# Optimization experiments

Hardware: AMD Instinct MI355X
Metric: run time of the kernel (lower is better)

Reference implementation:

```python
import jax, jax.numpy as jnp
import numpy as np

N = 50000
E = 800000
H = 128

def _mlp_init(key, sizes, bias_flags):
    ws = []
    for i, (din, dout) in enumerate(zip(sizes[:-1], sizes[1:])):
        key, k1, k2 = jax.random.split(key, 3)
        lim = 1.0 / np.sqrt(din)
        W = jax.random.uniform(k1, (din, dout), jnp.float32, -lim, lim)
        ws.append(W)
        if bias_flags[i]:
            ws.append(jax.random.uniform(k2, (dout,), jnp.float32, -lim, lim))
    return key, ws

def setup_inputs() -> dict:
    key = jax.random.key(0)
    key, kh, kx, ke = jax.random.split(key, 4)
    h = jax.random.normal(kh, (N, H), jnp.float32)
    x = jax.random.normal(kx, (N, 3), jnp.float32)
    edge_index = jax.random.randint(ke, (2, E), 0, N, jnp.int64)
    # edge_mlp: Linear(2H+1, H), Linear(H, H), both with bias
    key, (W_e1, b_e1, W_e2, b_e2) = _mlp_init(key, [2 * H + 1, H, H], [True, True])
    # coord_mlp: Linear(H, H) with bias, Linear(H, 1) no bias
    key, (W_c1, b_c1, W_c2) = _mlp_init(key, [H, H, 1], [True, False])
    # node_mlp: Linear(2H, H), Linear(H, H), both with bias
    key, (W_n1, b_n1, W_n2, b_n2) = _mlp_init(key, [2 * H, H, H], [True, True])
    ln_g = jnp.ones((H,), jnp.float32)
    ln_b = jnp.zeros((H,), jnp.float32)
    return {"h": h, "x": x, "edge_index": edge_index,
            "W_e1": W_e1, "b_e1": b_e1, "W_e2": W_e2, "b_e2": b_e2,
            "W_c1": W_c1, "b_c1": b_c1, "W_c2": W_c2,
            "W_n1": W_n1, "b_n1": b_n1, "W_n2": W_n2, "b_n2": b_n2,
            "ln_g": ln_g, "ln_b": ln_b}

def reference(h, x, edge_index, W_e1, b_e1, W_e2, b_e2, W_c1, b_c1, W_c2,
              W_n1, b_n1, W_n2, b_n2, ln_g, ln_b):
    row, col = edge_index[0], edge_index[1]
    coord_diff = x[row] - x[col]                       # [E, 3]
    dist = jnp.linalg.norm(coord_diff, axis=1, keepdims=True)  # [E, 1]
    radial = dist ** 2
    edge_input = jnp.concatenate([h[row], h[col], radial], axis=1)  # [E, 2H+1]
    m_ij = jax.nn.silu(jax.nn.silu(edge_input @ W_e1 + b_e1) @ W_e2 + b_e2)  # [E, H]
    force_scalar = jnp.tanh(jax.nn.silu(m_ij @ W_c1 + b_c1) @ W_c2) * 0.1    # [E, 1]
    norm_diff = coord_diff / (dist + 1e-8)
    force_vector = norm_diff * force_scalar            # [E, 3]
    x_new = x + jax.ops.segment_sum(force_vector, row, num_segments=N)
    m_i = jax.ops.segment_sum(m_ij, row, num_segments=N)  # [N, H]
    node_input = jnp.concatenate([h, m_i], axis=1)     # [N, 2H]
    h_res = h + jax.nn.silu(node_input @ W_n1 + b_n1) @ W_n2 + b_n2
    mu = jnp.mean(h_res, axis=-1, keepdims=True)
    var = jnp.var(h_res, axis=-1, keepdims=True)
    h_new = (h_res - mu) / jnp.sqrt(var + 1e-5) * ln_g + ln_b
    return (h_new, x_new)
```

## Files before the change

### kernel.cpp

```cpp
#include <hip/hip_runtime.h>
#include <hip/hip_bf16.h>

#define NN 50000
#define NE 800000
#define HH 128
#define SCAN_NB 196

typedef short s16x8 __attribute__((ext_vector_type(8)));
typedef float f32x4 __attribute__((ext_vector_type(4)));
typedef unsigned int u32x4 __attribute__((ext_vector_type(4)));
typedef __bf16 bf16x2 __attribute__((ext_vector_type(2)));

__device__ __forceinline__ float u2f(unsigned int v) {
    float f;
    __builtin_memcpy(&f, &v, 4);
    return f;
}
__device__ __forceinline__ float bf2f(unsigned short u) {
    return u2f(((unsigned int)u) << 16);
}
__device__ __forceinline__ unsigned short f2bf_sw(float f) {
    unsigned int x;
    __builtin_memcpy(&x, &f, 4);
    unsigned int r = (x + 0x7fffu + ((x >> 16) & 1u)) >> 16;
    return (unsigned short)r;
}
__device__ __forceinline__ unsigned int f2bf_pk(float a, float b) {
#if __has_builtin(__builtin_amdgcn_cvt_pk_bf16_f32)
    bf16x2 p = __builtin_amdgcn_cvt_pk_bf16_f32(a, b);
    unsigned int u;
    __builtin_memcpy(&u, &p, 4);
    return u;
#else
    return (unsigned int)f2bf_sw(a) | ((unsigned int)f2bf_sw(b) << 16);
#endif
}
__device__ __forceinline__ unsigned short f2bf(float a) {
#if __has_builtin(__builtin_amdgcn_cvt_pk_bf16_f32)
    return (unsigned short)(f2bf_pk(a, a) & 0xffffu);
#else
    return f2bf_sw(a);
#endif
}
__device__ __forceinline__ float silu(float v) {
    return v * __builtin_amdgcn_rcpf(1.f + __expf(-v));
}

__global__ void prep_kernel(
    const float* __restrict__ W_e1, const float* __restrict__ W_e2,
    const float* __restrict__ W_c1, const float* __restrict__ W_n1,
    const float* __restrict__ W_n2, const int* __restrict__ eidx,
    unsigned short* __restrict__ PWT, unsigned short* __restrict__ W2T,
    unsigned short* __restrict__ Wc1T, unsigned short* __restrict__ Wn1T,
    unsigned short* __restrict__ Wn2T, int* __restrict__ counts) {
    int idx = blockIdx.x * 256 + threadIdx.x;
    if (idx < 32768) {
        int cp = idx >> 7, k = idx & 127;
        int srow = (cp < 128) ? k : (128 + k);
        PWT[idx] = f2bf(W_e1[srow * 128 + (cp & 127)]);
    } else if (idx < 49152) {
        int i = idx - 32768, n = i >> 7, k = i & 127;
        W2T[i] = f2bf(W_e2[k * 128 + n]);
    } else if (idx < 65536) {
        int i = idx - 49152, n = i >> 7, k = i & 127;
        Wc1T[i] = f2bf(W_c1[k * 128 + n]);
    } else if (idx < 98304) {
        int i = idx - 65536, n = i >> 8, k = i & 255;
        Wn1T[i] = f2bf(W_n1[k * 128 + n]);
    } else if (idx < 114688) {
        int i = idx - 98304, n = i >> 7, k = i & 127;
        Wn2T[i] = f2bf(W_n2[k * 128 + n]);
    } else if (idx < 114688 + NE) {
        int e = idx - 114688;
        int r = eidx[e];
        r = r < 0 ? 0 : (r >= NN ? NN - 1 : r);
        atomicAdd(&counts[r], 1);
    }
}

__global__ void k_partial(const int* __restrict__ counts, int* __restrict__ partials) {
    __shared__ int sm[256];
    int idx = blockIdx.x * 256 + threadIdx.x;
    sm[threadIdx.x] = idx < NN ? counts[idx] : 0;
    __syncthreads();
    for (int s = 128; s > 0; s >>= 1) {
        if (threadIdx.x < s) sm[threadIdx.x] += sm[threadIdx.x + s];
        __syncthreads();
    }
    if (threadIdx.x == 0) partials[blockIdx.x] = sm[0];
}
__global__ void k_scanp(const int* __restrict__ partials, int* __restrict__ scanp) {
    __shared__ int sm[256];
    int t = threadIdx.x;
    int v = t < SCAN_NB ? partials[t] : 0;
    sm[t] = v;
    __syncthreads();
    for (int d = 1; d < 256; d <<= 1) {
        int add = t >= d ? sm[t - d] : 0;
        __syncthreads();
        sm[t] += add;
        __syncthreads();
    }
    scanp[t] = sm[t] - v;
}
__global__ void k_offsets(const int* __restrict__ counts, const int* __restrict__ scanp,
                          int* __restrict__ offsets) {
    __shared__ int sm[256];
    int t = threadIdx.x, idx = blockIdx.x * 256 + t;
    int v = idx < NN ? counts[idx] : 0;
    sm[t] = v;
    __syncthreads();
    for (int d = 1; d < 256; d <<= 1) {
        int add = t >= d ? sm[t - d] : 0;
        __syncthreads();
        sm[t] += add;
        __syncthreads();
    }
    if (idx < NN) offsets[idx] = sm[t] - v + scanp[blockIdx.x];
}

__global__ void k_fill(const int* __restrict__ eidx, const int* __restrict__ offsets,
                       int* __restrict__ cursor, unsigned int* __restrict__ rc) {
    int e = blockIdx.x * 256 + threadIdx.x;
    if (e >= NE) return;
    int r = eidx[e];
    int c = eidx[NE + e];
    r = r < 0 ? 0 : (r >= NN ? NN - 1 : r);
    c = c < 0 ? 0 : (c >= NN ? NN - 1 : c);
    int slot = offsets[r] + atomicAdd(&cursor[r], 1);
    rc[slot] = (unsigned int)r | ((unsigned int)c << 16);
}

__global__ __launch_bounds__(256, 4) void pgemm(
    const float* __restrict__ h, const unsigned short* __restrict__ PWT,
    const float* __restrict__ b1,
    float* __restrict__ P1, unsigned short* __restrict__ P2b) {
    __shared__ unsigned short Alds[64 * 136];
    const int tid = threadIdx.x;
    const int n0 = blockIdx.x * 64;

#pragma unroll
    for (int j = 0; j < 4; j++) {
        int idx = tid + j * 256;
        int e = idx >> 4, ch = idx & 15;
        int node = n0 + e;
        if (node >= NN) node = NN - 1;
        const f32x4* p = (const f32x4*)&h[node * 128 + ch * 8];
        f32x4 a = p[0], b = p[1];
        u32x4 s;
        s[0] = f2bf_pk(a[0], a[1]);
        s[1] = f2bf_pk(a[2], a[3]);
        s[2] = f2bf_pk(b[0], b[1]);
        s[3] = f2bf_pk(b[2], b[3]);
        *(u32x4*)&Alds[e * 136 + ch * 8] = s;
    }
    __syncthreads();

    const int lane = tid & 63;
    const int w = tid >> 6;
    const int ln15 = lane & 15;
    const int q8 = (lane >> 4) * 8, q4 = (lane >> 4) * 4;
    const int cbase = w * 64;

    f32x4 acc[4][4];
#pragma unroll
    for (int et = 0; et < 4; et++)
#pragma unroll
        for (int nt = 0; nt < 4; nt++) acc[et][nt] = (f32x4){0.f, 0.f, 0.f, 0.f};
#pragma unroll
    for (int kk = 0; kk < 4; kk++) {
        int k0 = kk * 32 + q8;
        s16x8 a[4], b[4];
#pragma unroll
        for (int et = 0; et < 4; et++)
            a[et] = *(const s16x8*)&Alds[(et * 16 + ln15) * 136 + k0];
#pragma unroll
        for (int nt = 0; nt < 4; nt++)
            b[nt] = *(const s16x8*)&PWT[(cbase + nt * 16 + ln15) * 128 + k0];
#pragma unroll
        for (int et = 0; et < 4; et++)
#pragma unroll
            for (int nt = 0; nt < 4; nt++)
                acc[et][nt] = __builtin_amdgcn_mfma_f32_16x16x32_bf16(
                    a[et], b[nt], acc[et][nt], 0, 0, 0);
    }
#pragma unroll
    for (int nt = 0; nt < 4; nt++) {
        int cp = cbase + nt * 16 + ln15;
        bool top = cp < 128;
        int col = cp & 127;
        float badd = top ? b1[col] : 0.f;
#pragma unroll
        for (int et = 0; et < 4; et++)
#pragma unroll
            for (int r = 0; r < 4; r++) {
                int row = et * 16 + q4 + r;
                int node = n0 + row;
                if (node >= NN) node = NN - 1;
                float v = acc[et][nt][r] + badd;
                if (top) P1[(size_t)node * 128 + col] = v;
                else     P2b[(size_t)node * 128 + col] = f2bf(v);
            }
    }
}

__global__ __launch_bounds__(256, 4) void edge_kernel(
    const float* __restrict__ P1, const unsigned short* __restrict__ P2b,
    const float* __restrict__ x, const unsigned int* __restrict__ rc,
    const float* __restrict__ W1full,
    const unsigned short* __restrict__ W2T, const float* __restrict__ b2,
    const unsigned short* __restrict__ Wc1T, const float* __restrict__ bc1,
    const float* __restrict__ wc2,
    float* __restrict__ m_i, float* __restrict__ x_acc) {
    __shared__ unsigned short mid1[64 * 132];
    __shared__ float wls[128];
    __shared__ float rad[64], ndx[64], ndy[64], ndz[64], fsum[64];
    __shared__ int rowA[64], colA[64];

    const int tid = threadIdx.x;
    const int nwg = NE / 64;
    const int qq = nwg >> 3, r8 = nwg & 7;
    const int xcd = blockIdx.x & 7, pos = blockIdx.x >> 3;
    const int swz = (xcd < r8 ? xcd * (qq + 1) : r8 * (qq + 1) + (xcd - r8) * qq) + pos;
    const int e0 = swz * 64;

    if (tid < 64) {
        unsigned int pk = rc[e0 + tid];
        int r = pk & 0xffff, c = pk >> 16;
        rowA[tid] = r; colA[tid] = c;
        float dx = x[r * 3 + 0] - x[c * 3 + 0];
        float dy = x[r * 3 + 1] - x[c * 3 + 1];
        float dz = x[r * 3 + 2] - x[c * 3 + 2];
        float d2 = dx * dx + dy * dy + dz * dz;
        float dist = sqrtf(d2);
        float inv = __builtin_amdgcn_rcpf(dist + 1e-8f);
        rad[tid] = d2;
        ndx[tid] = dx * inv; ndy[tid] = dy * inv; ndz[tid] = dz * inv;
        fsum[tid] = 0.f;
    } else if (tid >= 128 && tid < 256) {
        int c = tid - 128;
        wls[c] = W1full[256 * 128 + c];
    }
    __syncthreads();

#pragma unroll
    for (int j = 0; j < 4; j++) {
        int idx = tid + j * 256;
        int e = idx >> 4, ch = idx & 15;
        int r = rowA[e], c = colA[e];
        const f32x4* q1 = (const f32x4*)&P1[(size_t)r * 128 + ch * 8];
        f32x4 a0 = q1[0], a1 = q1[1];
        u32x4 c01 = *(const u32x4*)&P2b[(size_t)c * 128 + ch * 8];
        float rd = rad[e];
        int colb = ch * 8;
        u32x4 s;
#pragma unroll
        for (int t = 0; t < 2; t++) {
            float v0 = a0[t * 2]     + u2f(c01[t] << 16)        + rd * wls[colb + t * 2];
            float v1 = a0[t * 2 + 1] + u2f(c01[t] & 0xffff0000u) + rd * wls[colb + t * 2 + 1];
            s[t] = f2bf_pk(silu(v0), silu(v1));
        }
#pragma unroll
        for (int t = 0; t < 2; t++) {
            int cc = colb + 4 + t * 2;
            float v0 = a1[t * 2]     + u2f(c01[t + 2] << 16)        + rd * wls[cc];
            float v1 = a1[t * 2 + 1] + u2f(c01[t + 2] & 0xffff0000u) + rd * wls[cc + 1];
            s[t + 2] = f2bf_pk(silu(v0), silu(v1));
        }
        *(u32x4*)&mid1[e * 132 + ch * 8] = s;
    }
    __syncthreads();

    const int lane = tid & 63;
    const int w = tid >> 6;
    const int ln15 = lane & 15;
    const int q8 = (lane >> 4) * 8, q4 = (lane >> 4) * 4;
    const int nbase = w * 32;

    f32x4 acc[4][2];

#pragma unroll
    for (int et = 0; et < 4; et++)
#pragma unroll
        for (int nt = 0; nt < 2; nt++) acc[et][nt] = (f32x4){0.f, 0.f, 0.f, 0.f};
#pragma unroll
    for (int kk = 0; kk < 4; kk++) {
        int k0 = kk * 32 + q8;
        s16x8 a[4], b[2];
#pragma unroll
        for (int et = 0; et < 4; et++)
            a[et] = *(const s16x8*)&mid1[(et * 16 + ln15) * 132 + k0];
#pragma unroll
        for (int nt = 0; nt < 2; nt++)
            b[nt] = *(const s16x8*)&W2T[(nbase + nt * 16 + ln15) * 128 + k0];
#pragma unroll
        for (int et = 0; et < 4; et++)
#pragma unroll
            for (int nt = 0; nt < 2; nt++)
                acc[et][nt] = __builtin_amdgcn_mfma_f32_16x16x32_bf16(
                    a[et], b[nt], acc[et][nt], 0, 0, 0);
    }
    __syncthreads();
    unsigned short* mid2 = mid1;
#pragma unroll
    for (int nt = 0; nt < 2; nt++) {
        int col = nbase + nt * 16 + ln15;
        float bias = b2[col];
#pragma unroll
        for (int et = 0; et < 4; et++)
#pragma unroll
            for (int r = 0; r < 4; r++) {
                int row = et * 16 + q4 + r;
                mid2[row * 132 + col] = f2bf(silu(acc[et][nt][r] + bias));
            }
    }
    __syncthreads();

#pragma unroll
    for (int et = 0; et < 4; et++)
#pragma unroll
        for (int nt = 0; nt < 2; nt++) acc[et][nt] = (f32x4){0.f, 0.f, 0.f, 0.f};
#pragma unroll
    for (int kk = 0; kk < 4; kk++) {
        int k0 = kk * 32 + q8;
        s16x8 a[4], b[2];
#pragma unroll
        for (int et = 0; et < 4; et++)
            a[et] = *(const s16x8*)&mid2[(et * 16 + ln15) * 132 + k0];
#pragma unroll
        for (int nt = 0; nt < 2; nt++)
            b[nt] = *(const s16x8*)&Wc1T[(nbase + nt * 16 + ln15) * 128 + k0];
#pragma unroll
        for (int et = 0; et < 4; et++)
#pragma unroll
            for (int nt = 0; nt < 2; nt++)
                acc[et][nt] = __builtin_amdgcn_mfma_f32_16x16x32_bf16(
                    a[et], b[nt], acc[et][nt], 0, 0, 0);
    }

    {
        int cp2 = (tid & 63) * 2;
        int g = tid >> 6;
        int r0 = g * 16;
        float a0 = 0.f, a1 = 0.f;
        int cur = rowA[r0];
        for (int row = r0; row < r0 + 16; row++) {
            int rn = rowA[row];
            if (rn != cur) {
                atomicAdd(&m_i[(size_t)cur * 128 + cp2], a0);
                atomicAdd(&m_i[(size_t)cur * 128 + cp2 + 1], a1);
                a0 = 0.f; a1 = 0.f;
                cur = rn;
            }
            unsigned int v = *(const unsigned int*)&mid2[row * 132 + cp2];
            a0 += u2f(v << 16);
            a1 += u2f(v & 0xffff0000u);
        }
        atomicAdd(&m_i[(size_t)cur * 128 + cp2], a0);
        atomicAdd(&m_i[(size_t)cur * 128 + cp2 + 1], a1);
    }

    {
        float part[4][4];
#pragma unroll
        for (int et = 0; et < 4; et++)
#pragma unroll
            for (int r = 0; r < 4; r++) part[et][r] = 0.f;
#pragma unroll
        for (int nt = 0; nt < 2; nt++) {
            int col = nbase + nt * 16 + ln15;
            float bias = bc1[col];
            float w2 = wc2[col];
#pragma unroll
            for (int et = 0; et < 4; et++)
#pragma unroll
                for (int r = 0; r < 4; r++)
                    part[et][r] += silu(acc[et][nt][r] + bias) * w2;
        }
#pragma unroll
        for (int et = 0; et < 4; et++)
#pragma unroll
            for (int r = 0; r < 4; r++) {
                float p = part[et][r];
                p += __shfl_xor(p, 8, 16);
                p += __shfl_xor(p, 4, 16);
                p += __shfl_xor(p, 2, 16);
                p += __shfl_xor(p, 1, 16);
                if (ln15 == 0) atomicAdd(&fsum[et * 16 + q4 + r], p);
            }
    }
    __syncthreads();
    if (tid < 64) {
        float fs = tanhf(fsum[tid]) * 0.1f;
        ndx[tid] *= fs; ndy[tid] *= fs; ndz[tid] *= fs;
    }
    __syncthreads();
    if (tid < 64) {
        bool head = (tid == 0) || (rowA[tid] != rowA[tid - 1]);
        if (head) {
            int rn = rowA[tid];
            float ax = 0.f, ay = 0.f, az = 0.f;
            for (int j = tid; j < 64 && rowA[j] == rn; j++) {
                ax += ndx[j]; ay += ndy[j]; az += ndz[j];
            }
            atomicAdd(&x_acc[rn * 3 + 0], ax);
            atomicAdd(&x_acc[rn * 3 + 1], ay);
            atomicAdd(&x_acc[rn * 3 + 2], az);
        }
    }
}

__global__ __launch_bounds__(256, 4) void node_kernel(
    const float* __restrict__ h, const float* __restrict__ m_i,
    const float* __restrict__ x, const float* __restrict__ x_acc,
    const unsigned short* __restrict__ Wn1T, const float* __restrict__ bn1,
    const unsigned short* __restrict__ Wn2T, const float* __restrict__ bn2,
    const float* __restrict__ ln_g, const float* __restrict__ ln_b,
    float* __restrict__ out_h, float* __restrict__ out_x) {
    __shared__ unsigned short Alds[64 * 264];
    unsigned short* mid1 = Alds;
    float* tile = (float*)Alds;

    const int tid = threadIdx.x;
    const int n0 = blockIdx.x * 64;

    if (tid < 192) {
        int i = n0 * 3 + tid;
        if (i < NN * 3) out_x[i] = x[i] + x_acc[i];
    }

#pragma unroll
    for (int i = 0; i < 8; i++) {
        int idx = tid + i * 256;
        int hr = idx >> 4, ch = idx & 15;
        int e = hr >> 1, half = hr & 1;
        int node = n0 + e;
        if (node >= NN) node = NN - 1;
        const float* src = half ? &m_i[(size_t)node * 128 + ch * 8]
                                : &h[(size_t)node * 128 + ch * 8];
        const f32x4* sp = (const f32x4*)src;
        f32x4 f0 = sp[0], f1 = sp[1];
        u32x4 s;
        s[0] = f2bf_pk(f0[0], f0[1]);
        s[1] = f2bf_pk(f0[2], f0[3]);
        s[2] = f2bf_pk(f1[0], f1[1]);
        s[3] = f2bf_pk(f1[2], f1[3]);
        *(u32x4*)&Alds[e * 264 + half * 128 + ch * 8] = s;
    }
    __syncthreads();

    const int lane = tid & 63;
    const int w = tid >> 6;
    const int ln15 = lane & 15;
    const int q8 = (lane >> 4) * 8, q4 = (lane >> 4) * 4;
    const int nbase = w * 32;

    f32x4 acc[4][2];

#pragma unroll
    for (int et = 0; et < 4; et++)
#pragma unroll
        for (int nt = 0; nt < 2; nt++) acc[et][nt] = (f32x4){0.f, 0.f, 0.f, 0.f};
#pragma unroll
    for (int kk = 0; kk < 8; kk++) {
        int k0 = kk * 32 + q8;
        s16x8 a[4], b[2];
#pragma unroll
        for (int et = 0; et < 4; et++)
            a[et] = *(const s16x8*)&Alds[(et * 16 + ln15) * 264 + k0];
#pragma unroll
        for (int nt = 0; nt < 2; nt++)
            b[nt] = *(const s16x8*)&Wn1T[(nbase + nt * 16 + ln15) * 256 + k0];
#pragma unroll
        for (int et = 0; et < 4; et++)
#pragma unroll
            for (int nt = 0; nt < 2; nt++)
                acc[et][nt] = __builtin_amdgcn_mfma_f32_16x16x32_bf16(
                    a[et], b[nt], acc[et][nt], 0, 0, 0);
    }
    __syncthreads();
#pragma unroll
    for (int nt = 0; nt < 2; nt++) {
        int col = nbase + nt * 16 + ln15;
        float bias = bn1[col];
#pragma unroll
        for (int et = 0; et < 4; et++)
#pragma unroll
            for (int r = 0; r < 4; r++) {
                int row = et * 16 + q4 + r;
                mid1[row * 132 + col] = f2bf(silu(acc[et][nt][r] + bias));
            }
    }
    __syncthreads();

#pragma unroll
    for (int et = 0; et < 4; et++)
#pragma unroll
        for (int nt = 0; nt < 2; nt++) acc[et][nt] = (f32x4){0.f, 0.f, 0.f, 0.f};
#pragma unroll
    for (int kk = 0; kk < 4; kk++) {
        int k0 = kk * 32 + q8;
        s16x8 a[4], b[2];
#pragma unroll
        for (int et = 0; et < 4; et++)
            a[et] = *(const s16x8*)&mid1[(et * 16 + ln15) * 132 + k0];
#pragma unroll
        for (int nt = 0; nt < 2; nt++)
            b[nt] = *(const s16x8*)&Wn2T[(nbase + nt * 16 + ln15) * 128 + k0];
#pragma unroll
        for (int et = 0; et < 4; et++)
#pragma unroll
            for (int nt = 0; nt < 2; nt++)
                acc[et][nt] = __builtin_amdgcn_mfma_f32_16x16x32_bf16(
                    a[et], b[nt], acc[et][nt], 0, 0, 0);
    }
    __syncthreads();
#pragma unroll
    for (int nt = 0; nt < 2; nt++) {
        int col = nbase + nt * 16 + ln15;
        float bias = bn2[col];
#pragma unroll
        for (int et = 0; et < 4; et++)
#pragma unroll
            for (int r = 0; r < 4; r++) {
                int row = et * 16 + q4 + r;
                int node = n0 + row;
                int nclamp = node >= NN ? NN - 1 : node;
                float v = acc[et][nt][r] + bias + h[(size_t)nclamp * 128 + col];
                tile[row * 132 + col] = v;
            }
    }
    __syncthreads();

    {
        int row = tid >> 2;
        int q = tid & 3;
        float s = 0.f, s2 = 0.f;
#pragma unroll
        for (int c = 0; c < 32; c++) {
            float v = tile[row * 132 + q + c * 4];
            s += v; s2 += v * v;
        }
        s += __shfl_xor(s, 1, 4);  s2 += __shfl_xor(s2, 1, 4);
        s += __shfl_xor(s, 2, 4);  s2 += __shfl_xor(s2, 2, 4);
        float mean = s * (1.f / 128.f);
        float var = s2 * (1.f / 128.f) - mean * mean;
        float rs = rsqrtf(var + 1e-5f);
        int node = n0 + row;
        if (node < NN) {
#pragma unroll
            for (int c = 0; c < 32; c++) {
                int col = q + c * 4;
                float v = (tile[row * 132 + col] - mean) * rs * ln_g[col] + ln_b[col];
                out_h[(size_t)node * 128 + col] = v;
            }
        }
    }
}

extern "C" void kernel_launch(void* const* d_in, const int* in_sizes, int n_in,
                              void* d_out, int out_size, void* d_ws, size_t ws_size,
                              hipStream_t stream) {
    const float* h    = (const float*)d_in[0];
    const float* x    = (const float*)d_in[1];
    const int* eidx   = (const int*)d_in[2];
    const float* W_e1 = (const float*)d_in[3];
    const float* b_e1 = (const float*)d_in[4];
    const float* W_e2 = (const float*)d_in[5];
    const float* b_e2 = (const float*)d_in[6];
    const float* W_c1 = (const float*)d_in[7];
    const float* b_c1 = (const float*)d_in[8];
    const float* W_c2 = (const float*)d_in[9];
    const float* W_n1 = (const float*)d_in[10];
    const float* b_n1 = (const float*)d_in[11];
    const float* W_n2 = (const float*)d_in[12];
    const float* b_n2 = (const float*)d_in[13];
    const float* ln_g = (const float*)d_in[14];
    const float* ln_b = (const float*)d_in[15];

    float* out_h = (float*)d_out;
    float* out_x = out_h + NN * HH;

    char* ws = (char*)d_ws;
    float* m_i    = (float*)ws;
    float* x_acc  = (float*)(ws + 25600000);
    int* counts   = (int*)(ws + 26200000);
    int* cursor   = (int*)(ws + 26400000);
    int* offsets  = (int*)(ws + 26600000);
    int* partials = (int*)(ws + 26800000);
    int* scanp    = (int*)(ws + 26801024);
    unsigned int* rc = (unsigned int*)(ws + 26802048);
    float* P1 = (float*)(ws + 30002048);
    unsigned short* P2b = (unsigned short*)(ws + 55602048);
    unsigned short* PWT  = (unsigned short*)(ws + 81202048);
    unsigned short* W2T  = (unsigned short*)(ws + 81267584);
    unsigned short* Wc1T = (unsigned short*)(ws + 81300352);
    unsigned short* Wn1T = (unsigned short*)(ws + 81333120);
    unsigned short* Wn2T = (unsigned short*)(ws + 81398656);

    hipMemsetAsync(ws, 0, 26800000, stream);

    prep_kernel<<<(114688 + NE + 255) / 256, 256, 0, stream>>>(
        W_e1, W_e2, W_c1, W_n1, W_n2, eidx, PWT, W2T, Wc1T, Wn1T, Wn2T, counts);
    k_partial<<<SCAN_NB, 256, 0, stream>>>(counts, partials);
    k_scanp<<<1, 256, 0, stream>>>(partials, scanp);
    k_offsets<<<SCAN_NB, 256, 0, stream>>>(counts, scanp, offsets);
    k_fill<<<(NE + 255) / 256, 256, 0, stream>>>(eidx, offsets, cursor, rc);
    pgemm<<<(NN + 63) / 64, 256, 0, stream>>>(h, PWT, b_e1, P1, P2b);

    edge_kernel<<<NE / 64, 256, 0, stream>>>(P1, P2b, x, rc, W_e1, W2T, b_e2,
                                             Wc1T, b_c1, W_c2, m_i, x_acc);
    node_kernel<<<(NN + 63) / 64, 256, 0, stream>>>(
        h, m_i, x, x_acc, Wn1T, b_n1, Wn2T, b_n2, ln_g, ln_b, out_h, out_x);
}
```

Measured before the change: 443.4 us.

## Process two 64-edge tiles per block with interleaved staging and MFMA layers

Each edge-kernel workgroup now handles 128 edges as two 64-edge tiles in separate LDS buffers. The gather/stage step of one tile and the matmul/epilogue steps of the other are interleaved so that global gathers and LDS writes can overlap MFMA work, and barriers are shared across both tiles. This doubles LDS use and accumulator registers per block, which may lower occupancy under the existing launch bounds, and halves the grid size.

Result: slower. 550.8 us (+24.2%).

```diff
diff --git a/kernel.cpp b/kernel.cpp
--- a/kernel.cpp
+++ b/kernel.cpp
@@ -204,6 +204,153 @@
     }
 }
 
+
+__device__ __forceinline__ void stage_tile(
+    unsigned short* mid, int base, int tid,
+    const int* rowL, const int* colL, const float* radL, const float* wls,
+    const float* __restrict__ P1, const unsigned short* __restrict__ P2b) {
+#pragma unroll
+    for (int j = 0; j < 4; j++) {
+        int idx = tid + j * 256;
+        int e = idx >> 4, ch = idx & 15;
+        int r = rowL[base + e], c = colL[base + e];
+        const f32x4* q1 = (const f32x4*)&P1[(size_t)r * 128 + ch * 8];
+        f32x4 a0 = q1[0], a1 = q1[1];
+        u32x4 c01 = *(const u32x4*)&P2b[(size_t)c * 128 + ch * 8];
+        float rd = radL[base + e];
+        int colb = ch * 8;
+        u32x4 s;
+#pragma unroll
+        for (int t = 0; t < 2; t++) {
+            float v0 = a0[t * 2]     + u2f(c01[t] << 16)         + rd * wls[colb + t * 2];
+            float v1 = a0[t * 2 + 1] + u2f(c01[t] & 0xffff0000u) + rd * wls[colb + t * 2 + 1];
+            s[t] = f2bf_pk(silu(v0), silu(v1));
+        }
+#pragma unroll
+        for (int t = 0; t < 2; t++) {
+            int cc = colb + 4 + t * 2;
+            float v0 = a1[t * 2]     + u2f(c01[t + 2] << 16)         + rd * wls[cc];
+            float v1 = a1[t * 2 + 1] + u2f(c01[t + 2] & 0xffff0000u) + rd * wls[cc + 1];
+            s[t + 2] = f2bf_pk(silu(v0), silu(v1));
+        }
+        *(u32x4*)&mid[e * 132 + colb] = s;
+    }
+}
+
+__device__ __forceinline__ void mm_layer(
+    f32x4 (&acc)[4][2], const unsigned short* mid,
+    const unsigned short* __restrict__ wt, int tid) {
+    const int lane = tid & 63;
+    const int w = tid >> 6;
+    const int ln15 = lane & 15;
+    const int q8 = (lane >> 4) * 8;
+    const int nbase = w * 32;
+#pragma unroll
+    for (int et = 0; et < 4; et++)
+#pragma unroll
+        for (int nt = 0; nt < 2; nt++) acc[et][nt] = (f32x4){0.f, 0.f, 0.f, 0.f};
+#pragma unroll
+    for (int kk = 0; kk < 4; kk++) {
+        int k0 = kk * 32 + q8;
+        s16x8 a[4], b[2];
+#pragma unroll
+        for (int et = 0; et < 4; et++)
+            a[et] = *(const s16x8*)&mid[(et * 16 + ln15) * 132 + k0];
+#pragma unroll
+        for (int nt = 0; nt < 2; nt++)
+            b[nt] = *(const s16x8*)&wt[(nbase + nt * 16 + ln15) * 128 + k0];
+#pragma unroll
+        for (int et = 0; et < 4; et++)
+#pragma unroll
+            for (int nt = 0; nt < 2; nt++)
+                acc[et][nt] = __builtin_amdgcn_mfma_f32_16x16x32_bf16(
+                    a[et], b[nt], acc[et][nt], 0, 0, 0);
+    }
+}
+
+__device__ __forceinline__ void write_mid2(
+    const f32x4 (&acc)[4][2], unsigned short* mid,
+    const float* __restrict__ b2, int tid) {
+    const int lane = tid & 63;
+    const int w = tid >> 6;
+    const int ln15 = lane & 15;
+    const int q4 = (lane >> 4) * 4;
+    const int nbase = w * 32;
+#pragma unroll
+    for (int nt = 0; nt < 2; nt++) {
+        int col = nbase + nt * 16 + ln15;
+        float bias = b2[col];
+#pragma unroll
+        for (int et = 0; et < 4; et++)
+#pragma unroll
+            for (int r = 0; r < 4; r++) {
+                int row = et * 16 + q4 + r;
+                mid[row * 132 + col] = f2bf(silu(acc[et][nt][r] + bias));
+            }
+    }
+}
+
+__device__ __forceinline__ void mi_reduce(
+    const unsigned short* mid, const int* rowL, int base, int tid,
+    float* __restrict__ m_i) {
+    int cp2 = (tid & 63) * 2;
+    int g = tid >> 6;
+    int r0g = g * 16;
+    float a0 = 0.f, a1 = 0.f;
+    int cur = rowL[base + r0g];
+    for (int row = r0g; row < r0g + 16; row++) {
+        int rn = rowL[base + row];
+        if (rn != cur) {
+            atomicAdd(&m_i[(size_t)cur * 128 + cp2], a0);
+            atomicAdd(&m_i[(size_t)cur * 128 + cp2 + 1], a1);
+            a0 = 0.f; a1 = 0.f;
+            cur = rn;
+        }
+        unsigned int v = *(const unsigned int*)&mid[row * 132 + cp2];
+        a0 += u2f(v << 16);
+        a1 += u2f(v & 0xffff0000u);
+    }
+    atomicAdd(&m_i[(size_t)cur * 128 + cp2], a0);
+    atomicAdd(&m_i[(size_t)cur * 128 + cp2 + 1], a1);
+}
+
+__device__ __forceinline__ void coord_epi(
+    const f32x4 (&acc)[4][2], const float* __restrict__ bc1,
+    const float* __restrict__ wc2, float* fsumL, int base, int tid) {
+    const int lane = tid & 63;
+    const int w = tid >> 6;
+    const int ln15 = lane & 15;
+    const int q4 = (lane >> 4) * 4;
+    const int nbase = w * 32;
+    float part[4][4];
+#pragma unroll
+    for (int et = 0; et < 4; et++)
+#pragma unroll
+        for (int r = 0; r < 4; r++) part[et][r] = 0.f;
+#pragma unroll
+    for (int nt = 0; nt < 2; nt++) {
+        int col = nbase + nt * 16 + ln15;
+        float bias = bc1[col];
+        float w2 = wc2[col];
+#pragma unroll
+        for (int et = 0; et < 4; et++)
+#pragma unroll
+            for (int r = 0; r < 4; r++)
+                part[et][r] += silu(acc[et][nt][r] + bias) * w2;
+    }
+#pragma unroll
+    for (int et = 0; et < 4; et++)
+#pragma unroll
+        for (int r = 0; r < 4; r++) {
+            float p = part[et][r];
+            p += __shfl_xor(p, 8, 16);
+            p += __shfl_xor(p, 4, 16);
+            p += __shfl_xor(p, 2, 16);
+            p += __shfl_xor(p, 1, 16);
+            if (ln15 == 0) atomicAdd(&fsumL[base + et * 16 + q4 + r], p);
+        }
+}
+
 __global__ __launch_bounds__(256, 4) void edge_kernel(
     const float* __restrict__ P1, const unsigned short* __restrict__ P2b,
     const float* __restrict__ x, const unsigned int* __restrict__ rc,
@@ -212,196 +359,93 @@
     const unsigned short* __restrict__ Wc1T, const float* __restrict__ bc1,
     const float* __restrict__ wc2,
     float* __restrict__ m_i, float* __restrict__ x_acc) {
-    __shared__ unsigned short mid1[64 * 132];
+    __shared__ unsigned short mid_A[64 * 132];
+    __shared__ unsigned short mid_B[64 * 132];
     __shared__ float wls[128];
-    __shared__ float rad[64], ndx[64], ndy[64], ndz[64], fsum[64];
-    __shared__ int rowA[64], colA[64];
+    __shared__ float radL[128], ndxL[128], ndyL[128], ndzL[128], fsumL[128];
+    __shared__ int rowL[128], colL[128];
 
     const int tid = threadIdx.x;
-    const int nwg = NE / 64;
+    const int nwg = NE / 128;
     const int qq = nwg >> 3, r8 = nwg & 7;
     const int xcd = blockIdx.x & 7, pos = blockIdx.x >> 3;
     const int swz = (xcd < r8 ? xcd * (qq + 1) : r8 * (qq + 1) + (xcd - r8) * qq) + pos;
-    const int e0 = swz * 64;
-
-    if (tid < 64) {
+    const int e0 = swz * 128;
+
+    if (tid < 128) {
         unsigned int pk = rc[e0 + tid];
         int r = pk & 0xffff, c = pk >> 16;
-        rowA[tid] = r; colA[tid] = c;
+        rowL[tid] = r; colL[tid] = c;
         float dx = x[r * 3 + 0] - x[c * 3 + 0];
         float dy = x[r * 3 + 1] - x[c * 3 + 1];
         float dz = x[r * 3 + 2] - x[c * 3 + 2];
         float d2 = dx * dx + dy * dy + dz * dz;
         float dist = sqrtf(d2);
         float inv = __builtin_amdgcn_rcpf(dist + 1e-8f);
-        rad[tid] = d2;
-        ndx[tid] = dx * inv; ndy[tid] = dy * inv; ndz[tid] = dz * inv;
-        fsum[tid] = 0.f;
-    } else if (tid >= 128 && tid < 256) {
+        radL[tid] = d2;
+        ndxL[tid] = dx * inv; ndyL[tid] = dy * inv; ndzL[tid] = dz * inv;
+        fsumL[tid] = 0.f;
+    } else {
         int c = tid - 128;
         wls[c] = W1full[256 * 128 + c];
     }
     __syncthreads();
 
-#pragma unroll
-    for (int j = 0; j < 4; j++) {
-        int idx = tid + j * 256;
-        int e = idx >> 4, ch = idx & 15;
-        int r = rowA[e], c = colA[e];
-        const f32x4* q1 = (const f32x4*)&P1[(size_t)r * 128 + ch * 8];
-        f32x4 a0 = q1[0], a1 = q1[1];
-        u32x4 c01 = *(const u32x4*)&P2b[(size_t)c * 128 + ch * 8];
-        float rd = rad[e];
-        int colb = ch * 8;
-        u32x4 s;
-#pragma unroll
-        for (int t = 0; t < 2; t++) {
-            float v0 = a0[t * 2]     + u2f(c01[t] << 16)        + rd * wls[colb + t * 2];
-            float v1 = a0[t * 2 + 1] + u2f(c01[t] & 0xffff0000u) + rd * wls[colb + t * 2 + 1];
-            s[t] = f2bf_pk(silu(v0), silu(v1));
-        }
-#pragma unroll
-        for (int t = 0; t < 2; t++) {
-            int cc = colb + 4 + t * 2;
-            float v0 = a1[t * 2]     + u2f(c01[t + 2] << 16)        + rd * wls[cc];
-            float v1 = a1[t * 2 + 1] + u2f(c01[t + 2] & 0xffff0000u) + rd * wls[cc + 1];
-            s[t + 2] = f2bf_pk(silu(v0), silu(v1));
-        }
-        *(u32x4*)&mid1[e * 132 + ch * 8] = s;
-    }
-    __syncthreads();
-
-    const int lane = tid & 63;
-    const int w = tid >> 6;
-    const int ln15 = lane & 15;
-    const int q8 = (lane >> 4) * 8, q4 = (lane >> 4) * 4;
-    const int nbase = w * 32;
-
-    f32x4 acc[4][2];
-
-#pragma unroll
-    for (int et = 0; et < 4; et++)
-#pragma unroll
-        for (int nt = 0; nt < 2; nt++) acc[et][nt] = (f32x4){0.f, 0.f, 0.f, 0.f};
-#pragma unroll
-    for (int kk = 0; kk < 4; kk++) {
-        int k0 = kk * 32 + q8;
-        s16x8 a[4], b[2];
-#pragma unroll
-        for (int et = 0; et < 4; et++)
-            a[et] = *(const s16x8*)&mid1[(et * 16 + ln15) * 132 + k0];
-#pragma unroll
-        for (int nt = 0; nt < 2; nt++)
-            b[nt] = *(const s16x8*)&W2T[(nbase + nt * 16 + ln15) * 128 + k0];
-#pragma unroll
-        for (int et = 0; et < 4; et++)
-#pragma unroll
-            for (int nt = 0; nt < 2; nt++)
-                acc[et][nt] = __builtin_amdgcn_mfma_f32_16x16x32_bf16(
-                    a[et], b[nt], acc[et][nt], 0, 0, 0);
-    }
-    __syncthreads();
-    unsigned short* mid2 = mid1;
-#pragma unroll
-    for (int nt = 0; nt < 2; nt++) {
-        int col = nbase + nt * 16 + ln15;
-        float bias = b2[col];
-#pragma unroll
-        for (int et = 0; et < 4; et++)
-#pragma unroll
-            for (int r = 0; r < 4; r++) {
-                int row = et * 16 + q4 + r;
-                mid2[row * 132 + col] = f2bf(silu(acc[et][nt][r] + bias));
+    f32x4 accA[4][2], accB[4][2];
+
+    stage_tile(mid_A, 0, tid, rowL, colL, radL, wls, P1, P2b);
+    __syncthreads();
+
+    mm_layer(accA, mid_A, W2T, tid);
+    stage_tile(mid_B, 64, tid, rowL, colL, radL, wls, P1, P2b);
+    __syncthreads();
+
+    mm_layer(accB, mid_B, W2T, tid);
+    write_mid2(accA, mid_A, b2, tid);
+    __syncthreads();
+
+    mm_layer(accA, mid_A, Wc1T, tid);
+    write_mid2(accB, mid_B, b2, tid);
+    __syncthreads();
+
+    mm_layer(accB, mid_B, Wc1T, tid);
+    mi_reduce(mid_A, rowL, 0, tid, m_i);
+    coord_epi(accA, bc1, wc2, fsumL, 0, tid);
+    __syncthreads();
+    if (tid < 64) {
+        float fs = tanhf(fsumL[tid]) * 0.1f;
+        ndxL[tid] *= fs; ndyL[tid] *= fs; ndzL[tid] *= fs;
+    }
+    __syncthreads();
+    if (tid < 64) {
+        bool head = (tid == 0) || (rowL[tid] != rowL[tid - 1]);
+        if (head) {
+            int rn = rowL[tid];
+            float ax = 0.f, ay = 0.f, az = 0.f;
+            for (int j = tid; j < 64 && rowL[j] == rn; j++) {
+                ax += ndxL[j]; ay += ndyL[j]; az += ndzL[j];
             }
-    }
-    __syncthreads();
-
-#pragma unroll
-    for (int et = 0; et < 4; et++)
-#pragma unroll
-        for (int nt = 0; nt < 2; nt++) acc[et][nt] = (f32x4){0.f, 0.f, 0.f, 0.f};
-#pragma unroll
-    for (int kk = 0; kk < 4; kk++) {
-        int k0 = kk * 32 + q8;
-        s16x8 a[4], b[2];
-#pragma unroll
-        for (int et = 0; et < 4; et++)
-            a[et] = *(const s16x8*)&mid2[(et * 16 + ln15) * 132 + k0];
-#pragma unroll
-        for (int nt = 0; nt < 2; nt++)
-            b[nt] = *(const s16x8*)&Wc1T[(nbase + nt * 16 + ln15) * 128 + k0];
-#pragma unroll
-        for (int et = 0; et < 4; et++)
-#pragma unroll
-            for (int nt = 0; nt < 2; nt++)
-                acc[et][nt] = __builtin_amdgcn_mfma_f32_16x16x32_bf16(
-                    a[et], b[nt], acc[et][nt], 0, 0, 0);
-    }
-
-    {
-        int cp2 = (tid & 63) * 2;
-        int g = tid >> 6;
-        int r0 = g * 16;
-        float a0 = 0.f, a1 = 0.f;
-        int cur = rowA[r0];
-        for (int row = r0; row < r0 + 16; row++) {
-            int rn = rowA[row];
-            if (rn != cur) {
-                atomicAdd(&m_i[(size_t)cur * 128 + cp2], a0);
-                atomicAdd(&m_i[(size_t)cur * 128 + cp2 + 1], a1);
-                a0 = 0.f; a1 = 0.f;
-                cur = rn;
-            }
-            unsigned int v = *(const unsigned int*)&mid2[row * 132 + cp2];
-            a0 += u2f(v << 16);
-            a1 += u2f(v & 0xffff0000u);
-        }
-        atomicAdd(&m_i[(size_t)cur * 128 + cp2], a0);
-        atomicAdd(&m_i[(size_t)cur * 128 + cp2 + 1], a1);
-    }
-
-    {
-        float part[4][4];
-#pragma unroll
-        for (int et = 0; et < 4; et++)
-#pragma unroll
-            for (int r = 0; r < 4; r++) part[et][r] = 0.f;
-#pragma unroll
-        for (int nt = 0; nt < 2; nt++) {
-            int col = nbase + nt * 16 + ln15;
-            float bias = bc1[col];
-            float w2 = wc2[col];
-#pragma unroll
-            for (int et = 0; et < 4; et++)
-#pragma unroll
-                for (int r = 0; r < 4; r++)
-                    part[et][r] += silu(acc[et][nt][r] + bias) * w2;
-        }
-#pragma unroll
-        for (int et = 0; et < 4; et++)
-#pragma unroll
-            for (int r = 0; r < 4; r++) {
-                float p = part[et][r];
-                p += __shfl_xor(p, 8, 16);
-                p += __shfl_xor(p, 4, 16);
-                p += __shfl_xor(p, 2, 16);
-                p += __shfl_xor(p, 1, 16);
-                if (ln15 == 0) atomicAdd(&fsum[et * 16 + q4 + r], p);
-            }
-    }
+            atomicAdd(&x_acc[rn * 3 + 0], ax);
+            atomicAdd(&x_acc[rn * 3 + 1], ay);
+            atomicAdd(&x_acc[rn * 3 + 2], az);
+        }
+    }
+
+    mi_reduce(mid_B, rowL, 64, tid, m_i);
+    coord_epi(accB, bc1, wc2, fsumL, 64, tid);
     __syncthreads();
     if (tid < 64) {
-        float fs = tanhf(fsum[tid]) * 0.1f;
-        ndx[tid] *= fs; ndy[tid] *= fs; ndz[tid] *= fs;
+        float fs = tanhf(fsumL[64 + tid]) * 0.1f;
+        ndxL[64 + tid] *= fs; ndyL[64 + tid] *= fs; ndzL[64 + tid] *= fs;
     }
     __syncthreads();
     if (tid < 64) {
-        bool head = (tid == 0) || (rowA[tid] != rowA[tid - 1]);
+        bool head = (tid == 0) || (rowL[64 + tid] != rowL[64 + tid - 1]);
         if (head) {
-            int rn = rowA[tid];
+            int rn = rowL[64 + tid];
             float ax = 0.f, ay = 0.f, az = 0.f;
-            for (int j = tid; j < 64 && rowA[j] == rn; j++) {
-                ax += ndx[j]; ay += ndy[j]; az += ndz[j];
+            for (int j = tid; j < 64 && rowL[64 + j] == rn; j++) {
+                ax += ndxL[64 + j]; ay += ndyL[64 + j]; az += ndzL[64 + j];
             }
             atomicAdd(&x_acc[rn * 3 + 0], ax);
             atomicAdd(&x_acc[rn * 3 + 1], ay);
@@ -608,8 +652,8 @@
     k_fill<<<(NE + 255) / 256, 256, 0, stream>>>(eidx, offsets, cursor, rc);
     pgemm<<<(NN + 63) / 64, 256, 0, stream>>>(h, PWT, b_e1, P1, P2b);
 
-    edge_kernel<<<NE / 64, 256, 0, stream>>>(P1, P2b, x, rc, W_e1, W2T, b_e2,
-                                             Wc1T, b_c1, W_c2, m_i, x_acc);
+    edge_kernel<<<NE / 128, 256, 0, stream>>>(P1, P2b, x, rc, W_e1, W2T, b_e2,
+                                              Wc1T, b_c1, W_c2, m_i, x_acc);
     node_kernel<<<(NN + 63) / 64, 256, 0, stream>>>(
         h, m_i, x, x_acc, Wn1T, b_n1, Wn2T, b_n2, ln_g, ln_b, out_h, out_x);
 }
```
